# Kernel optimization log

Measured on AMD Instinct MI355X. Metric: run time of the kernel, lower is better.

Reference implementation:

```python
import jax, jax.numpy as jnp
import numpy as np

HW, B, C, NH, NC, HF, WF = 2500, 2, 256, 8, 6, 64, 176
DFF = 4 * C
EPS = 1e-5

def _layernorm(x, g, b):
    m = x.mean(-1, keepdims=True)
    v = ((x - m) ** 2).mean(-1, keepdims=True)
    return (x - m) / jnp.sqrt(v + EPS) * g + b

def _mha(q, kv, in_w, in_b, ow, ob):
    # q: [L,B,C], kv: [S,B,C] (batch_first=False, torch nn.MultiheadAttention)
    L, Bq, Cq = q.shape
    S = kv.shape[0]
    Dh = Cq // NH
    qp = (q @ in_w[:Cq].T + in_b[:Cq]).reshape(L, Bq, NH, Dh)
    kp = (kv @ in_w[Cq:2 * Cq].T + in_b[Cq:2 * Cq]).reshape(S, Bq, NH, Dh)
    vp = (kv @ in_w[2 * Cq:].T + in_b[2 * Cq:]).reshape(S, Bq, NH, Dh)
    att = jnp.einsum('lbhd,sbhd->bhls', qp, kp) * (1.0 / np.sqrt(Dh))
    att = jax.nn.softmax(att, axis=-1)
    out = jnp.einsum('bhls,sbhd->lbhd', att, vp).reshape(L, Bq, Cq)
    return out @ ow.T + ob

def _grid_sample_zeros(feat, grid):
    # feat: [B,N,C,H,W], grid: [B,N,Q,2] in [-1,1]; bilinear, align_corners=False, zero padding
    Bb, N, Cc, Hf, Wf = feat.shape
    Q = grid.shape[2]
    x = (grid[..., 0] + 1.0) * (Wf / 2.0) - 0.5
    y = (grid[..., 1] + 1.0) * (Hf / 2.0) - 0.5
    x0 = jnp.floor(x); y0 = jnp.floor(y)
    wx = x - x0; wy = y - y0
    x0i = x0.astype(jnp.int32); y0i = y0.astype(jnp.int32)
    ff = feat.reshape(Bb, N, Cc, Hf * Wf)
    def corner(xi, yi, w):
        valid = (xi >= 0) & (xi < Wf) & (yi >= 0) & (yi < Hf)
        idx = jnp.clip(yi, 0, Hf - 1) * Wf + jnp.clip(xi, 0, Wf - 1)  # [B,N,Q]
        g = jnp.take_along_axis(ff, jnp.broadcast_to(idx[:, :, None, :], (Bb, N, Cc, Q)), axis=-1)
        return g * (w * valid)[:, :, None, :]
    return (corner(x0i, y0i, (1.0 - wx) * (1.0 - wy)) + corner(x0i + 1, y0i, wx * (1.0 - wy))
            + corner(x0i, y0i + 1, (1.0 - wx) * wy) + corner(x0i + 1, y0i + 1, wx * wy))

def _forward(bev_queries, prev_bev, image_feat, reference_points, camera_intrinsics, camera_extrinsics,
             in_proj_w, in_proj_b, out_proj_w, out_proj_b, tsa_norm_g, tsa_norm_b,
             sca_w, sca_b, sca_norm_g, sca_norm_b, ffn_w1, ffn_b1, ffn_w2, ffn_b2, ffn_norm_g, ffn_norm_b):
    # TSA (dropout is identity in eval)
    tsa_out = _mha(bev_queries, prev_bev, in_proj_w, in_proj_b, out_proj_w, out_proj_b)
    x = _layernorm(bev_queries + tsa_out, tsa_norm_g, tsa_norm_b)
    # SCA: ego->camera->image projection
    R = camera_extrinsics[:, :, :3, :3]            # [B,N,3,3]
    t = camera_extrinsics[:, :, :3, 3]             # [B,N,3]
    R_e2c = jnp.swapaxes(R, -1, -2)
    t_e2c = -jnp.einsum('bnij,bnj->bni', R_e2c, t)
    pts_cam = jnp.einsum('bnij,qj->bnqi', R_e2c, reference_points) + t_e2c[:, :, None, :]  # [B,N,Q,3]
    pts_img = jnp.einsum('bnij,bnqj->bnqi', camera_intrinsics, pts_cam)
    uv = pts_img[..., :2] / jnp.maximum(pts_img[..., 2:3], 1e-5)
    grid = jnp.stack([2.0 * uv[..., 0] / WF - 1.0, 2.0 * uv[..., 1] / HF - 1.0], axis=-1)  # [B,N,Q,2]
    Bq = bev_queries.shape[1]
    feat_r = image_feat.reshape(Bq, NC, C, HF, WF)
    sampled = _grid_sample_zeros(feat_r, grid).mean(axis=1)   # [B,C,Q]
    sampled = jnp.transpose(sampled, (2, 0, 1))               # [Q,B,C]
    sca_out = sampled @ sca_w.T + sca_b
    x = _layernorm(x + sca_out, sca_norm_g, sca_norm_b)
    # FFN (torch nn.GELU default = exact erf)
    h = jax.nn.gelu(x @ ffn_w1 + ffn_b1, approximate=False)
    ffn_out = h @ ffn_w2 + ffn_b2
    return _layernorm(x + ffn_out, ffn_norm_g, ffn_norm_b)

def setup_inputs():
    key = jax.random.key(0)
    ks = jax.random.split(key, 16)
    f = jnp.float32
    s = 0.02
    return {
        'bev_queries': jax.random.normal(ks[0], (HW, B, C), f),
        'prev_bev': jax.random.normal(ks[1], (HW, B, C), f),
        'image_feat': jax.random.normal(ks[2], (B * NC, C, HF, WF), f),
        'reference_points': jax.random.normal(ks[3], (HW, 3), f) * 20.0,
        'camera_intrinsics': jax.random.normal(ks[4], (B, NC, 3, 3), f),
        'camera_extrinsics': jax.random.normal(ks[5], (B, NC, 4, 4), f),
        'spatial_shapes': jnp.array([[HF, WF]], jnp.int32),
        'in_proj_w': jax.random.normal(ks[6], (3 * C, C), f) * s,
        'in_proj_b': jnp.zeros((3 * C,), f),
        'out_proj_w': jax.random.normal(ks[7], (C, C), f) * s,
        'out_proj_b': jnp.zeros((C,), f),
        'tsa_norm_g': jnp.ones((C,), f), 'tsa_norm_b': jnp.zeros((C,), f),
        'sca_w': jax.random.normal(ks[8], (C, C), f) * s,
        'sca_b': jnp.zeros((C,), f),
        'sca_norm_g': jnp.ones((C,), f), 'sca_norm_b': jnp.zeros((C,), f),
        'ffn_w1': jax.random.normal(ks[9], (C, DFF), f) * s,
        'ffn_b1': jnp.zeros((DFF,), f),
        'ffn_w2': jax.random.normal(ks[10], (DFF, C), f) * s,
        'ffn_b2': jnp.zeros((C,), f),
        'ffn_norm_g': jnp.ones((C,), f), 'ffn_norm_b': jnp.zeros((C,), f),
    }

def reference(bev_queries, prev_bev, image_feat, reference_points, camera_intrinsics, camera_extrinsics,
              in_proj_w, in_proj_b, out_proj_w, out_proj_b, tsa_norm_g, tsa_norm_b,
              sca_w, sca_b, sca_norm_g, sca_norm_b, ffn_w1, ffn_b1, ffn_w2, ffn_b2, ffn_norm_g, ffn_norm_b,
              spatial_shapes):
    return _forward(bev_queries, prev_bev, image_feat, reference_points, camera_intrinsics, camera_extrinsics,
                    in_proj_w, in_proj_b, out_proj_w, out_proj_b, tsa_norm_g, tsa_norm_b,
                    sca_w, sca_b, sca_norm_g, sca_norm_b, ffn_w1, ffn_b1, ffn_w2, ffn_b2, ffn_norm_g, ffn_norm_b)
```

## Files before the change

### kernel.cpp

```cpp
#include <hip/hip_runtime.h>

typedef unsigned short u16;
typedef __attribute__((ext_vector_type(8))) __bf16 bf8_t;
typedef __attribute__((ext_vector_type(4))) float f4_t;

union bf8u { u16 u[8]; bf8_t v; uint4 q; };

__device__ __forceinline__ float bf2f(u16 v) {
  return __uint_as_float(((unsigned int)v) << 16);
}
__device__ __forceinline__ u16 f2bf(float f) {
  union { __bf16 h; u16 u; } c;
  c.h = (__bf16)f;
  return c.u;
}
__device__ __forceinline__ float bflo(unsigned int w) { return __uint_as_float(w << 16); }
__device__ __forceinline__ float bfhi(unsigned int w) { return __uint_as_float(w & 0xFFFF0000u); }
__device__ __forceinline__ float ldf1(const void* p, size_t i, int isf32) {
  return isf32 ? ((const float*)p)[i] : bf2f(((const u16*)p)[i]);
}
__device__ __forceinline__ unsigned int cvtpk(float lo, float hi) {
  unsigned int w;
  asm("v_cvt_pk_bf16_f32 %0, %1, %2" : "=v"(w) : "v"(lo), "v"(hi));
  return w;
}

#define LQ    2500
#define LQP   2560
#define BB    2
#define CC    256
#define NCC   6
#define HFF   64
#define WFF   176
#define DFF   1024
#define MROWS 5000

#define WB_UV   256
#define WB_WQKV 240256
#define WB_WOP  633472
#define WB_WSC  764544
#define WB_WF1  895616
#define WB_WF2  1419904
#define WB_S1   1944192
#define WB_S2   (WB_S1 + 2621440)
#define WB_S3   (WB_S2 + 2621440)
#define WB_VT   (WB_S3 + 2621440)
#define WB_H    WB_S2

__global__ void detect_k(const u16* __restrict__ rp, int* __restrict__ flag) {
  int bad = 0;
  for (int i = threadIdx.x; i < 7500; i += 64) {
    float v = bf2f(rp[i]);
    if (!(fabsf(v) < 1e6f)) bad = 1;
  }
  int anybad = __any(bad);
  if (threadIdx.x == 0) flag[0] = anybad ? 1 : 0;
}

struct WDesc {
  const void* src[3];
  u16* dst[3];
  int n[3];
};
__global__ __launch_bounds__(256) void cvtw_k(WDesc d, u16* __restrict__ vtp,
    const void* __restrict__ refp, const void* __restrict__ intr,
    const void* __restrict__ extr, float* __restrict__ uv,
    const int* __restrict__ flag) {
  const int df = flag[0];
  const int i = blockIdx.y;
  if (i == 4) {
    for (int idx = blockIdx.x * 256 + threadIdx.x; idx < BB * NCC * LQ; idx += gridDim.x * 256) {
      const int bc = idx / LQ;
      const int q = idx - bc * LQ;
      float R[3][3], tv[3], Kc[3][3], p[3];
#pragma unroll
      for (int a = 0; a < 3; ++a) {
#pragma unroll
        for (int j = 0; j < 3; ++j) {
          R[a][j] = ldf1(extr, bc*16 + a*4 + j, df);
          Kc[a][j] = ldf1(intr, bc*9 + a*3 + j, df);
        }
        tv[a] = ldf1(extr, bc*16 + a*4 + 3, df);
      }
#pragma unroll
      for (int j = 0; j < 3; ++j) p[j] = ldf1(refp, q*3 + j, df) - tv[j];
      float pc[3];
#pragma unroll
      for (int a = 0; a < 3; ++a) pc[a] = R[0][a]*p[0] + R[1][a]*p[1] + R[2][a]*p[2];
      float im[3];
#pragma unroll
      for (int a = 0; a < 3; ++a) im[a] = Kc[a][0]*pc[0] + Kc[a][1]*pc[1] + Kc[a][2]*pc[2];
      const float z = fmaxf(im[2], 1e-5f);
      uv[(size_t)idx*2 + 0] = im[0] / z - 0.5f;
      uv[(size_t)idx*2 + 1] = im[1] / z - 0.5f;
    }
    return;
  }
  if (i == 3) {
    const int n = 512 * (LQP - LQ);
    for (int j = blockIdx.x * 256 + threadIdx.x; j < n; j += gridDim.x * 256) {
      const int row = j / (LQP - LQ), col = LQ + j % (LQP - LQ);
      vtp[(size_t)row * LQP + col] = 0;
    }
    return;
  }
  const int n = d.n[i];
  for (int j = blockIdx.x * 256 + threadIdx.x; j < n; j += gridDim.x * 256) {
    if (df) {
      const float4 r = ((const float4*)d.src[i])[j];
      const unsigned int lo = (unsigned int)f2bf(r.x) | ((unsigned int)f2bf(r.y) << 16);
      const unsigned int hi = (unsigned int)f2bf(r.z) | ((unsigned int)f2bf(r.w) << 16);
      ((uint2*)d.dst[i])[j] = make_uint2(lo, hi);
    } else {
      ((uint2*)d.dst[i])[j] = ((const uint2*)d.src[i])[j];
    }
  }
}

__global__ __launch_bounds__(256) void trans_k(
    const void* __restrict__ s0, u16* __restrict__ d0,
    const void* __restrict__ s1, u16* __restrict__ d1,
    const int* __restrict__ flag)
{
  __shared__ u16 tile[64][66];
  const int df = flag[0];
  const void* src; u16* dst; int Ks, Ns;
  if (blockIdx.y == 0) { src = s0; dst = d0; Ks = 256;  Ns = 1024; }
  else                 { src = s1; dst = d1; Ks = 1024; Ns = 256;  }
  const int ntn = Ns >> 6;
  const int kx = blockIdx.x / ntn, nx = blockIdx.x % ntn;
  const int k0 = kx * 64, n0 = nx * 64;
  const int t = threadIdx.x;
  const int col = t & 63, rq = t >> 6;
#pragma unroll
  for (int i = 0; i < 16; ++i) {
    const int r = i * 4 + rq;
    tile[col][r] = f2bf(ldf1(src, (size_t)(k0 + r) * Ns + n0 + col, df));
  }
  __syncthreads();
#pragma unroll
  for (int i = 0; i < 16; ++i) {
    const int n = i * 4 + rq;
    dst[(size_t)(n0 + n) * Ks + k0 + col] = tile[n][col];
  }
}

template<int KTPL, int ACT, int NT>
__global__ __launch_bounds__(64) void gemm_nl(
    const u16* __restrict__ Xv, const u16* __restrict__ W,
    const void* __restrict__ bias,
    u16* __restrict__ Y, int M, int N, const int* __restrict__ flag)
{
  const int df = flag[0];
  const int lane = threadIdx.x;
  const int ln15 = lane & 15, l4 = lane >> 4;
  const int m0 = blockIdx.x * 32, n0 = blockIdx.y * (NT * 16);
  const int am0 = min(m0 + ln15, M - 1);
  const int am1 = min(m0 + 16 + ln15, M - 1);

  f4_t acc[2][NT];
#pragma unroll
  for (int g = 0; g < 2; ++g)
#pragma unroll
    for (int nt = 0; nt < NT; ++nt) acc[g][nt] = (f4_t){0.f, 0.f, 0.f, 0.f};

#pragma unroll 8
  for (int k0 = 0; k0 < KTPL; k0 += 32) {
    bf8u a0, a1;
    a0.q = *(const uint4*)(Xv + (size_t)am0 * KTPL + k0 + l4 * 8);
    a1.q = *(const uint4*)(Xv + (size_t)am1 * KTPL + k0 + l4 * 8);
#pragma unroll
    for (int nt = 0; nt < NT; ++nt) {
      bf8u b;
      b.q = *(const uint4*)&W[(size_t)(n0 + nt * 16 + ln15) * KTPL + k0 + l4 * 8];
      acc[0][nt] = __builtin_amdgcn_mfma_f32_16x16x32_bf16(a0.v, b.v, acc[0][nt], 0, 0, 0);
      acc[1][nt] = __builtin_amdgcn_mfma_f32_16x16x32_bf16(a1.v, b.v, acc[1][nt], 0, 0, 0);
    }
  }
#pragma unroll
  for (int g = 0; g < 2; ++g) {
#pragma unroll
    for (int nt = 0; nt < NT; ++nt) {
      const int gn = n0 + nt * 16 + ln15;
      const float bv = ldf1(bias, gn, df);
#pragma unroll
      for (int r = 0; r < 4; ++r) {
        const int gm = m0 + g * 16 + l4 * 4 + r;
        if (gm < M) {
          float x = acc[g][nt][r] + bv;
          if (ACT) x = 0.5f * x * (1.f + erff(x * 0.70710678118654752f));
          Y[(size_t)gm * N + gn] = f2bf(x);
        }
      }
    }
  }
}

template<int KT, int RES, int TOOUT>
__global__ __launch_bounds__(256) void gemm_ln(
    const u16* __restrict__ Xv, const u16* __restrict__ W,
    const void* __restrict__ bias, const void* __restrict__ resv,
    const void* __restrict__ gw, const void* __restrict__ bw,
    void* __restrict__ Yv, int M, const int* __restrict__ flag)
{
  __shared__ float sR[4][32];
  const int df = flag[0];
  const int t = threadIdx.x;
  const int lane = t & 63, wn = t >> 6;
  const int ln15 = lane & 15, l4 = lane >> 4;
  const int m0 = blockIdx.x * 32;
  const int am0 = min(m0 + ln15, M - 1);
  const int am1 = min(m0 + 16 + ln15, M - 1);

  f4_t acc[2][4];
#pragma unroll
  for (int g = 0; g < 2; ++g)
#pragma unroll
    for (int nt = 0; nt < 4; ++nt) acc[g][nt] = (f4_t){0.f, 0.f, 0.f, 0.f};

#pragma unroll 8
  for (int k0 = 0; k0 < KT; k0 += 32) {
    bf8u a0, a1;
    a0.q = *(const uint4*)(Xv + (size_t)am0 * KT + k0 + l4 * 8);
    a1.q = *(const uint4*)(Xv + (size_t)am1 * KT + k0 + l4 * 8);
#pragma unroll
    for (int nt = 0; nt < 4; ++nt) {
      bf8u b;
      b.q = *(const uint4*)&W[(size_t)(wn * 64 + nt * 16 + ln15) * KT + k0 + l4 * 8];
      acc[0][nt] = __builtin_amdgcn_mfma_f32_16x16x32_bf16(a0.v, b.v, acc[0][nt], 0, 0, 0);
      acc[1][nt] = __builtin_amdgcn_mfma_f32_16x16x32_bf16(a1.v, b.v, acc[1][nt], 0, 0, 0);
    }
  }
  float x[2][4][4];
#pragma unroll
  for (int g = 0; g < 2; ++g)
#pragma unroll
    for (int nt = 0; nt < 4; ++nt) {
      const int gn = wn * 64 + nt * 16 + ln15;
      const float bv = ldf1(bias, gn, df);
#pragma unroll
      for (int r = 0; r < 4; ++r) {
        const int gm = m0 + g * 16 + l4 * 4 + r;
        float xx = acc[g][nt][r] + bv;
        const size_t ri = (size_t)min(gm, M - 1) * CC + gn;
        if (RES == 1)      xx += bf2f(((const u16*)resv)[ri]);
        else if (RES == 2) xx += ldf1(resv, ri, df);
        x[g][nt][r] = xx;
      }
    }
#pragma unroll
  for (int g = 0; g < 2; ++g) {
    float ps[4];
#pragma unroll
    for (int r = 0; r < 4; ++r) {
      ps[r] = x[g][0][r] + x[g][1][r] + x[g][2][r] + x[g][3][r];
#pragma unroll
      for (int o = 1; o < 16; o <<= 1) ps[r] += __shfl_xor(ps[r], o);
    }
    if (ln15 == 0) {
#pragma unroll
      for (int r = 0; r < 4; ++r) sR[wn][g * 16 + l4 * 4 + r] = ps[r];
    }
  }
  __syncthreads();
  float mean[2][4];
#pragma unroll
  for (int g = 0; g < 2; ++g)
#pragma unroll
    for (int r = 0; r < 4; ++r) {
      const int row = g * 16 + l4 * 4 + r;
      mean[g][r] = (sR[0][row] + sR[1][row] + sR[2][row] + sR[3][row]) * 0.00390625f;
    }
  __syncthreads();
#pragma unroll
  for (int g = 0; g < 2; ++g) {
    float pq[4];
#pragma unroll
    for (int r = 0; r < 4; ++r) {
      float d0 = x[g][0][r] - mean[g][r], d1 = x[g][1][r] - mean[g][r];
      float d2 = x[g][2][r] - mean[g][r], d3 = x[g][3][r] - mean[g][r];
      pq[r] = d0*d0 + d1*d1 + d2*d2 + d3*d3;
#pragma unroll
      for (int o = 1; o < 16; o <<= 1) pq[r] += __shfl_xor(pq[r], o);
    }
    if (ln15 == 0) {
#pragma unroll
      for (int r = 0; r < 4; ++r) sR[wn][g * 16 + l4 * 4 + r] = pq[r];
    }
  }
  __syncthreads();
  float rstd[2][4];
#pragma unroll
  for (int g = 0; g < 2; ++g)
#pragma unroll
    for (int r = 0; r < 4; ++r) {
      const int row = g * 16 + l4 * 4 + r;
      const float v = (sR[0][row] + sR[1][row] + sR[2][row] + sR[3][row]) * 0.00390625f;
      rstd[g][r] = rsqrtf(v + 1e-5f);
    }
#pragma unroll
  for (int g = 0; g < 2; ++g)
#pragma unroll
    for (int nt = 0; nt < 4; ++nt) {
      const int gn = wn * 64 + nt * 16 + ln15;
      const float gg = ldf1(gw, gn, df);
      const float be = ldf1(bw, gn, df);
#pragma unroll
      for (int r = 0; r < 4; ++r) {
        const int gm = m0 + g * 16 + l4 * 4 + r;
        if (gm < M) {
          const float y = (x[g][nt][r] - mean[g][r]) * rstd[g][r] * gg + be;
          if (TOOUT && df) ((float*)Yv)[(size_t)gm * CC + gn] = y;
          else             ((u16*)Yv)[(size_t)gm * CC + gn] = f2bf(y);
        }
      }
    }
}

__global__ __launch_bounds__(64) void gemm_qkv(
    const void* __restrict__ Xq, const void* __restrict__ Xkv,
    const u16* __restrict__ Wqkv, const void* __restrict__ bias,
    u16* __restrict__ Qo, u16* __restrict__ Ko, u16* __restrict__ Vt,
    const int* __restrict__ flag)
{
  const int df = flag[0];
  const int lane = threadIdx.x;
  const int ln15 = lane & 15, l4 = lane >> 4;
  const int which = blockIdx.y >> 2;
  const int n0 = (blockIdx.y & 3) * 64;
  const void* Xv = (which == 0) ? Xq : Xkv;
  const u16* W = Wqkv + (size_t)which * 65536;
  const int m0 = blockIdx.x * 32;
  const int am0 = min(m0 + ln15, MROWS - 1);
  const int am1 = min(m0 + 16 + ln15, MROWS - 1);

  f4_t acc[2][4];
#pragma unroll
  for (int g = 0; g < 2; ++g)
#pragma unroll
    for (int nt = 0; nt < 4; ++nt) acc[g][nt] = (f4_t){0.f, 0.f, 0.f, 0.f};

#pragma unroll 8
  for (int k0 = 0; k0 < CC; k0 += 32) {
    bf8u a0, a1;
    if (df) {
      const float* p0 = (const float*)Xv + (size_t)am0 * CC + k0 + l4 * 8;
      float4 r0 = *(const float4*)p0, r1 = *(const float4*)(p0 + 4);
      a0.u[0]=f2bf(r0.x); a0.u[1]=f2bf(r0.y); a0.u[2]=f2bf(r0.z); a0.u[3]=f2bf(r0.w);
      a0.u[4]=f2bf(r1.x); a0.u[5]=f2bf(r1.y); a0.u[6]=f2bf(r1.z); a0.u[7]=f2bf(r1.w);
      const float* p1 = (const float*)Xv + (size_t)am1 * CC + k0 + l4 * 8;
      float4 r2 = *(const float4*)p1, r3 = *(const float4*)(p1 + 4);
      a1.u[0]=f2bf(r2.x); a1.u[1]=f2bf(r2.y); a1.u[2]=f2bf(r2.z); a1.u[3]=f2bf(r2.w);
      a1.u[4]=f2bf(r3.x); a1.u[5]=f2bf(r3.y); a1.u[6]=f2bf(r3.z); a1.u[7]=f2bf(r3.w);
    } else {
      a0.q = *(const uint4*)((const u16*)Xv + (size_t)am0 * CC + k0 + l4 * 8);
      a1.q = *(const uint4*)((const u16*)Xv + (size_t)am1 * CC + k0 + l4 * 8);
    }
#pragma unroll
    for (int nt = 0; nt < 4; ++nt) {
      bf8u b;
      b.q = *(const uint4*)&W[(size_t)(n0 + nt * 16 + ln15) * CC + k0 + l4 * 8];
      acc[0][nt] = __builtin_amdgcn_mfma_f32_16x16x32_bf16(a0.v, b.v, acc[0][nt], 0, 0, 0);
      acc[1][nt] = __builtin_amdgcn_mfma_f32_16x16x32_bf16(a1.v, b.v, acc[1][nt], 0, 0, 0);
    }
  }
#pragma unroll
  for (int g = 0; g < 2; ++g) {
#pragma unroll
    for (int nt = 0; nt < 4; ++nt) {
      const int gn = n0 + nt * 16 + ln15;
      const float bv = ldf1(bias, which * 256 + gn, df);
#pragma unroll
      for (int r = 0; r < 4; ++r) {
        const int gm = m0 + g * 16 + l4 * 4 + r;
        if (gm < MROWS) {
          const float x = acc[g][nt][r] + bv;
          if (which == 2) {
            const int tt = gm >> 1;
            const int tx = tt & 63;
            const int tp = (tx & 35) | ((tx & 12) << 1) | ((tx & 16) >> 2);
            Vt[(size_t)(gn + (gm & 1) * 256) * LQP + ((tt & ~63) | tp)] = f2bf(x);
          } else {
            u16* Y = (which == 0) ? Qo : Ko;
            Y[(size_t)gm * CC + gn] = f2bf(x);
          }
        }
      }
    }
  }
}

#define TPW 10
__global__ __launch_bounds__(256) void attn_mf(
    const u16* __restrict__ Qw, const u16* __restrict__ Kw,
    const u16* __restrict__ Vt, u16* __restrict__ Ow)
{
  __shared__ float sO[4][32][33];
  __shared__ float sM[4][32];
  __shared__ float sL[4][32];
  const int t = threadIdx.x;
  const int lane = t & 63, w = t >> 6;
  const int ln15 = lane & 15, l4 = lane >> 4;
  const int q0 = blockIdx.x * 32;
  const int by = blockIdx.y;
  const int b = by >> 3, h = by & 7;
  const float SCL2E = 0.25505654481f;

  bf8u aqA, aqB;
  {
    const int qra = min(q0 + ln15, LQ - 1);
    const int qrb = min(q0 + 16 + ln15, LQ - 1);
    bf8u qr;
    qr.q = *(const uint4*)&Qw[((size_t)qra * BB + b) * CC + h * 32 + l4 * 8];
#pragma unroll
    for (int i = 0; i < 8; ++i) aqA.u[i] = f2bf(bf2f(qr.u[i]) * SCL2E);
    qr.q = *(const uint4*)&Qw[((size_t)qrb * BB + b) * CC + h * 32 + l4 * 8];
#pragma unroll
    for (int i = 0; i < 8; ++i) aqB.u[i] = f2bf(bf2f(qr.u[i]) * SCL2E);
  }

  f4_t oaccA[2], oaccB[2];
  oaccA[0] = (f4_t){0.f,0.f,0.f,0.f}; oaccA[1] = (f4_t){0.f,0.f,0.f,0.f};
  oaccB[0] = (f4_t){0.f,0.f,0.f,0.f}; oaccB[1] = (f4_t){0.f,0.f,0.f,0.f};
  float mA = -1e30f, lA = 0.f;
  float mB = -1e30f, lB = 0.f;

  const int kt0 = w * TPW;
  const u16* Kbase = &Kw[(size_t)b * CC + h * 32 + l4 * 8];
  const u16* Vbase = &Vt[(size_t)(by * 32 + ln15) * LQP + l4 * 8];

  bf8u bkn[4];
#pragma unroll
  for (int nt = 0; nt < 4; ++nt)
    bkn[nt].q = *(const uint4*)&Kbase[(size_t)(kt0 * 64 + nt * 16 + ln15) * CC];

  for (int kt = kt0; kt < kt0 + TPW; ++kt) {
    const int kb = kt * 64;
    bf8u av[2][2];
#pragma unroll
    for (int m = 0; m < 2; ++m)
#pragma unroll
      for (int dt = 0; dt < 2; ++dt)
        av[m][dt].q = *(const uint4*)&Vbase[(size_t)(dt * 16) * LQP + kb + m * 32];
    f4_t svA[4], svB[4];
    __builtin_amdgcn_s_setprio(1);
#pragma unroll
    for (int nt = 0; nt < 4; ++nt) {
      f4_t z = (f4_t){0.f,0.f,0.f,0.f};
      svA[nt] = __builtin_amdgcn_mfma_f32_16x16x32_bf16(bkn[nt].v, aqA.v, z, 0, 0, 0);
      f4_t z2 = (f4_t){0.f,0.f,0.f,0.f};
      svB[nt] = __builtin_amdgcn_mfma_f32_16x16x32_bf16(bkn[nt].v, aqB.v, z2, 0, 0, 0);
    }
    __builtin_amdgcn_s_setprio(0);
    if (kt + 1 < kt0 + TPW) {
#pragma unroll
      for (int nt = 0; nt < 4; ++nt)
        bkn[nt].q = *(const uint4*)&Kbase[(size_t)(kb + 64 + nt * 16 + ln15) * CC];
    }
    float pA[4][4], pB[4][4];
    if (kb + 64 <= LQ) {
#pragma unroll
      for (int nt = 0; nt < 4; ++nt)
#pragma unroll
        for (int r = 0; r < 4; ++r) { pA[nt][r] = svA[nt][r]; pB[nt][r] = svB[nt][r]; }
    } else {
#pragma unroll
      for (int nt = 0; nt < 4; ++nt)
#pragma unroll
        for (int r = 0; r < 4; ++r) {
          const bool ok = (kb + nt * 16 + l4 * 4 + r < LQ);
          pA[nt][r] = ok ? svA[nt][r] : -1e30f;
          pB[nt][r] = ok ? svB[nt][r] : -1e30f;
        }
    }
    {
      const float thr = mA + 8.f;
      bool nd = false;
#pragma unroll
      for (int nt = 0; nt < 4; ++nt)
#pragma unroll
        for (int r = 0; r < 4; ++r) nd |= (pA[nt][r] > thr);
      if (__any(nd)) {
        const float x0 = fmaxf(fmaxf(pA[0][0], pA[0][1]), fmaxf(pA[0][2], pA[0][3]));
        const float x1 = fmaxf(fmaxf(pA[1][0], pA[1][1]), fmaxf(pA[1][2], pA[1][3]));
        const float x2 = fmaxf(fmaxf(pA[2][0], pA[2][1]), fmaxf(pA[2][2], pA[2][3]));
        const float x3 = fmaxf(fmaxf(pA[3][0], pA[3][1]), fmaxf(pA[3][2], pA[3][3]));
        float mloc = fmaxf(fmaxf(x0, x1), fmaxf(x2, x3));
        mloc = fmaxf(mloc, __shfl_xor(mloc, 16));
        mloc = fmaxf(mloc, __shfl_xor(mloc, 32));
        const float mn = fmaxf(mA, mloc);
        const float alpha = __builtin_amdgcn_exp2f(mA - mn);
        mA = mn;
        lA *= alpha;
#pragma unroll
        for (int r = 0; r < 4; ++r) { oaccA[0][r] *= alpha; oaccA[1][r] *= alpha; }
      }
      float s = 0.f;
#pragma unroll
      for (int nt = 0; nt < 4; ++nt)
#pragma unroll
        for (int r = 0; r < 4; ++r) {
          const float e = __builtin_amdgcn_exp2f(pA[nt][r] - mA);
          pA[nt][r] = e; s += e;
        }
      lA += s;
    }
    {
      const float thr = mB + 8.f;
      bool nd = false;
#pragma unroll
      for (int nt = 0; nt < 4; ++nt)
#pragma unroll
        for (int r = 0; r < 4; ++r) nd |= (pB[nt][r] > thr);
      if (__any(nd)) {
        const float x0 = fmaxf(fmaxf(pB[0][0], pB[0][1]), fmaxf(pB[0][2], pB[0][3]));
        const float x1 = fmaxf(fmaxf(pB[1][0], pB[1][1]), fmaxf(pB[1][2], pB[1][3]));
        const float x2 = fmaxf(fmaxf(pB[2][0], pB[2][1]), fmaxf(pB[2][2], pB[2][3]));
        const float x3 = fmaxf(fmaxf(pB[3][0], pB[3][1]), fmaxf(pB[3][2], pB[3][3]));
        float mloc = fmaxf(fmaxf(x0, x1), fmaxf(x2, x3));
        mloc = fmaxf(mloc, __shfl_xor(mloc, 16));
        mloc = fmaxf(mloc, __shfl_xor(mloc, 32));
        const float mn = fmaxf(mB, mloc);
        const float alpha = __builtin_amdgcn_exp2f(mB - mn);
        mB = mn;
        lB *= alpha;
#pragma unroll
        for (int r = 0; r < 4; ++r) { oaccB[0][r] *= alpha; oaccB[1][r] *= alpha; }
      }
      float s = 0.f;
#pragma unroll
      for (int nt = 0; nt < 4; ++nt)
#pragma unroll
        for (int r = 0; r < 4; ++r) {
          const float e = __builtin_amdgcn_exp2f(pB[nt][r] - mB);
          pB[nt][r] = e; s += e;
        }
      lB += s;
    }
    __builtin_amdgcn_s_setprio(1);
#pragma unroll
    for (int m = 0; m < 2; ++m) {
      bf8u pba, pbb;
      pba.q = make_uint4(cvtpk(pA[2*m][0], pA[2*m][1]),   cvtpk(pA[2*m][2], pA[2*m][3]),
                         cvtpk(pA[2*m+1][0], pA[2*m+1][1]), cvtpk(pA[2*m+1][2], pA[2*m+1][3]));
      pbb.q = make_uint4(cvtpk(pB[2*m][0], pB[2*m][1]),   cvtpk(pB[2*m][2], pB[2*m][3]),
                         cvtpk(pB[2*m+1][0], pB[2*m+1][1]), cvtpk(pB[2*m+1][2], pB[2*m+1][3]));
#pragma unroll
      for (int dt = 0; dt < 2; ++dt) {
        oaccA[dt] = __builtin_amdgcn_mfma_f32_16x16x32_bf16(av[m][dt].v, pba.v, oaccA[dt], 0, 0, 0);
        oaccB[dt] = __builtin_amdgcn_mfma_f32_16x16x32_bf16(av[m][dt].v, pbb.v, oaccB[dt], 0, 0, 0);
      }
    }
    __builtin_amdgcn_s_setprio(0);
  }
  lA += __shfl_xor(lA, 16);  lA += __shfl_xor(lA, 32);
  lB += __shfl_xor(lB, 16);  lB += __shfl_xor(lB, 32);
#pragma unroll
  for (int dt = 0; dt < 2; ++dt)
#pragma unroll
    for (int r = 0; r < 4; ++r) {
      sO[w][ln15][dt * 16 + l4 * 4 + r]      = oaccA[dt][r];
      sO[w][16 + ln15][dt * 16 + l4 * 4 + r] = oaccB[dt][r];
    }
  if (l4 == 0) {
    sM[w][ln15] = mA; sL[w][ln15] = lA;
    sM[w][16 + ln15] = mB; sL[w][16 + ln15] = lB;
  }
  __syncthreads();
#pragma unroll
  for (int i = t; i < 1024; i += 256) {
    const int row = i >> 5, col = i & 31;
    const float M = fmaxf(fmaxf(sM[0][row], sM[1][row]), fmaxf(sM[2][row], sM[3][row]));
    float l = 0.f, O = 0.f;
#pragma unroll
    for (int w4 = 0; w4 < 4; ++w4) {
      const float sc = __builtin_amdgcn_exp2f(sM[w4][row] - M);
      l += sc * sL[w4][row];
      O += sc * sO[w4][row][col];
    }
    const int q = q0 + row;
    if (q < LQ)
      Ow[((size_t)q * BB + b) * CC + h * 32 + col] = f2bf(O / l);
  }
}

__global__ __launch_bounds__(256) void samp_k(
    const void* __restrict__ feat, const float* __restrict__ uv,
    u16* __restrict__ S, const int* __restrict__ flag)
{
  const int df = flag[0];
  const int c = blockIdx.x;
  const int b = blockIdx.y / 5;
  const int ch = blockIdx.y % 5;
  const int qend = min((ch + 1) * 500, LQ);
  for (int q = ch * 500 + threadIdx.x; q < qend; q += 256) {
    float acc = 0.f;
#pragma unroll
    for (int cam = 0; cam < NCC; ++cam) {
      const int bc = b * NCC + cam;
      const float x = uv[((size_t)bc * LQ + q) * 2 + 0];
      const float y = uv[((size_t)bc * LQ + q) * 2 + 1];
      const float xf = floorf(x), yf = floorf(y);
      const int x0 = (int)xf, y0 = (int)yf;
      const float wx = x - xf, wy = y - yf;
      const size_t base = ((size_t)bc * CC + c) * (HFF * WFF);
      const bool vx0 = (x0 >= 0) & (x0 < WFF);
      const bool vx1 = (x0 + 1 >= 0) & (x0 + 1 < WFF);
      const bool vy0 = (y0 >= 0) & (y0 < HFF);
      const bool vy1 = (y0 + 1 >= 0) & (y0 + 1 < HFF);
      if (vy0) {
        const size_t rb = base + (size_t)y0 * WFF;
        if (vx0) acc += (1.f - wx) * (1.f - wy) * ldf1(feat, rb + x0, df);
        if (vx1) acc += wx * (1.f - wy) * ldf1(feat, rb + x0 + 1, df);
      }
      if (vy1) {
        const size_t rb = base + (size_t)(y0 + 1) * WFF;
        if (vx0) acc += (1.f - wx) * wy * ldf1(feat, rb + x0, df);
        if (vx1) acc += wx * wy * ldf1(feat, rb + x0 + 1, df);
      }
    }
    S[((size_t)q * BB + b) * CC + c] = f2bf(acc * (1.f / 6.f));
  }
}

extern "C" void kernel_launch(void* const* d_in, const int* in_sizes, int n_in,
                              void* d_out, int out_size, void* d_ws, size_t ws_size,
                              hipStream_t stream) {
  (void)in_sizes; (void)n_in; (void)out_size; (void)ws_size;
  char* base = (char*)d_ws;
  int* flag = (int*)base;
  float* UV = (float*)(base + WB_UV);
  u16* WQKV = (u16*)(base + WB_WQKV);
  u16* WOP  = (u16*)(base + WB_WOP);
  u16* WSC  = (u16*)(base + WB_WSC);
  u16* WF1  = (u16*)(base + WB_WF1);
  u16* WF2  = (u16*)(base + WB_WF2);
  u16* S1 = (u16*)(base + WB_S1);
  u16* S2 = (u16*)(base + WB_S2);
  u16* S3 = (u16*)(base + WB_S3);
  u16* VT = (u16*)(base + WB_VT);
  u16* H  = (u16*)(base + WB_H);

  detect_k<<<1, 64, 0, stream>>>((const u16*)d_in[3], flag);

  WDesc wd;
  wd.src[0] = d_in[7];  wd.dst[0] = WQKV; wd.n[0] = 49152;
  wd.src[1] = d_in[9];  wd.dst[1] = WOP;  wd.n[1] = 16384;
  wd.src[2] = d_in[13]; wd.dst[2] = WSC;  wd.n[2] = 16384;
  cvtw_k<<<dim3(128, 5), 256, 0, stream>>>(wd, VT, d_in[3], d_in[4], d_in[5], UV, flag);
  trans_k<<<dim3(64, 2), 256, 0, stream>>>(d_in[17], WF1, d_in[19], WF2, flag);

  gemm_qkv<<<dim3(157, 12), 64, 0, stream>>>(d_in[0], d_in[1], WQKV, d_in[8], S1, S2, VT, flag);

  attn_mf<<<dim3(79, 16), 256, 0, stream>>>(S1, S2, VT, S3);

  gemm_ln<256,2,0><<<157, 256, 0, stream>>>(S3, WOP, d_in[10], d_in[0], d_in[11], d_in[12], S2, MROWS, flag);

  samp_k<<<dim3(CC, BB * 5), 256, 0, stream>>>(d_in[2], UV, VT, flag);

  gemm_ln<256,1,0><<<157, 256, 0, stream>>>(VT, WSC, d_in[14], S2, d_in[15], d_in[16], S1, MROWS, flag);

  gemm_nl<256,1,4><<<dim3(157, 16), 64, 0, stream>>>(S1, WF1, d_in[18], H, MROWS, DFF, flag);
  gemm_ln<1024,1,1><<<157, 256, 0, stream>>>(H, WF2, d_in[20], S1, d_in[21], d_in[22], d_out, MROWS, flag);
}
```

Baseline: 453.9 us.

## Merge weight transpose into conversion kernel and co-schedule sampling with attention

Folds the FFN weight transpose kernel into the weight-conversion launch as an extra blockIdx.y slice. Also merges the independent bilinear camera sampling into the attention launch as extra blocks writing to a new workspace buffer SB, so the memory-bound gather can overlap with the compute-bound attention. This removes two kernel launches and lets both workloads share the GPU. The cost is that the sampling blocks now carry the attention kernel's shared-memory footprint, which may lower occupancy, and the workspace grows by one buffer.

```diff
diff --git a/kernel.cpp b/kernel.cpp
--- a/kernel.cpp
+++ b/kernel.cpp
@@ -45,6 +45,7 @@
 #define WB_S2   (WB_S1 + 2621440)
 #define WB_S3   (WB_S2 + 2621440)
 #define WB_VT   (WB_S3 + 2621440)
+#define WB_SB   (WB_VT + 2621440)
 #define WB_H    WB_S2
 
 __global__ void detect_k(const u16* __restrict__ rp, int* __restrict__ flag) {
@@ -65,9 +66,34 @@
 __global__ __launch_bounds__(256) void cvtw_k(WDesc d, u16* __restrict__ vtp,
     const void* __restrict__ refp, const void* __restrict__ intr,
     const void* __restrict__ extr, float* __restrict__ uv,
+    const void* __restrict__ tw1, u16* __restrict__ td1,
+    const void* __restrict__ tw2, u16* __restrict__ td2,
     const int* __restrict__ flag) {
   const int df = flag[0];
   const int i = blockIdx.y;
+  if (i == 5) {
+    __shared__ u16 tile[64][66];
+    const void* src; u16* dst; int Ks, Ns, bx;
+    if (blockIdx.x < 64) { src = tw1; dst = td1; Ks = 256;  Ns = 1024; bx = blockIdx.x; }
+    else                 { src = tw2; dst = td2; Ks = 1024; Ns = 256;  bx = blockIdx.x - 64; }
+    const int ntn = Ns >> 6;
+    const int kx = bx / ntn, nx = bx % ntn;
+    const int k0 = kx * 64, n0 = nx * 64;
+    const int t = threadIdx.x;
+    const int col = t & 63, rq = t >> 6;
+#pragma unroll
+    for (int ii = 0; ii < 16; ++ii) {
+      const int r = ii * 4 + rq;
+      tile[col][r] = f2bf(ldf1(src, (size_t)(k0 + r) * Ns + n0 + col, df));
+    }
+    __syncthreads();
+#pragma unroll
+    for (int ii = 0; ii < 16; ++ii) {
+      const int n = ii * 4 + rq;
+      dst[(size_t)(n0 + n) * Ks + k0 + col] = tile[n][col];
+    }
+    return;
+  }
   if (i == 4) {
     for (int idx = blockIdx.x * 256 + threadIdx.x; idx < BB * NCC * LQ; idx += gridDim.x * 256) {
       const int bc = idx / LQ;
@@ -114,34 +140,6 @@
     } else {
       ((uint2*)d.dst[i])[j] = ((const uint2*)d.src[i])[j];
     }
-  }
-}
-
-__global__ __launch_bounds__(256) void trans_k(
-    const void* __restrict__ s0, u16* __restrict__ d0,
-    const void* __restrict__ s1, u16* __restrict__ d1,
-    const int* __restrict__ flag)
-{
-  __shared__ u16 tile[64][66];
-  const int df = flag[0];
-  const void* src; u16* dst; int Ks, Ns;
-  if (blockIdx.y == 0) { src = s0; dst = d0; Ks = 256;  Ns = 1024; }
-  else                 { src = s1; dst = d1; Ks = 1024; Ns = 256;  }
-  const int ntn = Ns >> 6;
-  const int kx = blockIdx.x / ntn, nx = blockIdx.x % ntn;
-  const int k0 = kx * 64, n0 = nx * 64;
-  const int t = threadIdx.x;
-  const int col = t & 63, rq = t >> 6;
-#pragma unroll
-  for (int i = 0; i < 16; ++i) {
-    const int r = i * 4 + rq;
-    tile[col][r] = f2bf(ldf1(src, (size_t)(k0 + r) * Ns + n0 + col, df));
-  }
-  __syncthreads();
-#pragma unroll
-  for (int i = 0; i < 16; ++i) {
-    const int n = i * 4 + rq;
-    dst[(size_t)(n0 + n) * Ks + k0 + col] = tile[n][col];
   }
 }
 
@@ -391,18 +389,59 @@
 }
 
 #define TPW 10
-__global__ __launch_bounds__(256) void attn_mf(
+#define ATTN_BLOCKS (79 * 16)
+__global__ __launch_bounds__(256) void attn_samp(
     const u16* __restrict__ Qw, const u16* __restrict__ Kw,
-    const u16* __restrict__ Vt, u16* __restrict__ Ow)
+    const u16* __restrict__ Vt, u16* __restrict__ Ow,
+    const void* __restrict__ feat, const float* __restrict__ uv,
+    u16* __restrict__ SB, const int* __restrict__ flag)
 {
+  const int t = threadIdx.x;
+  if (blockIdx.x >= ATTN_BLOCKS) {
+    const int df = flag[0];
+    const int sid = blockIdx.x - ATTN_BLOCKS;
+    const int c = sid & 255;
+    const int yy = sid >> 8;
+    const int b = yy / 5;
+    const int ch = yy % 5;
+    const int qend = min((ch + 1) * 500, LQ);
+    for (int q = ch * 500 + t; q < qend; q += 256) {
+      float acc = 0.f;
+#pragma unroll
+      for (int cam = 0; cam < NCC; ++cam) {
+        const int bc = b * NCC + cam;
+        const float x = uv[((size_t)bc * LQ + q) * 2 + 0];
+        const float y = uv[((size_t)bc * LQ + q) * 2 + 1];
+        const float xf = floorf(x), yf = floorf(y);
+        const int x0 = (int)xf, y0 = (int)yf;
+        const float wx = x - xf, wy = y - yf;
+        const size_t base = ((size_t)bc * CC + c) * (HFF * WFF);
+        const bool vx0 = (x0 >= 0) & (x0 < WFF);
+        const bool vx1 = (x0 + 1 >= 0) & (x0 + 1 < WFF);
+        const bool vy0 = (y0 >= 0) & (y0 < HFF);
+        const bool vy1 = (y0 + 1 >= 0) & (y0 + 1 < HFF);
+        if (vy0) {
+          const size_t rb = base + (size_t)y0 * WFF;
+          if (vx0) acc += (1.f - wx) * (1.f - wy) * ldf1(feat, rb + x0, df);
+          if (vx1) acc += wx * (1.f - wy) * ldf1(feat, rb + x0 + 1, df);
+        }
+        if (vy1) {
+          const size_t rb = base + (size_t)(y0 + 1) * WFF;
+          if (vx0) acc += (1.f - wx) * wy * ldf1(feat, rb + x0, df);
+          if (vx1) acc += wx * wy * ldf1(feat, rb + x0 + 1, df);
+        }
+      }
+      SB[((size_t)q * BB + b) * CC + c] = f2bf(acc * (1.f / 6.f));
+    }
+    return;
+  }
   __shared__ float sO[4][32][33];
   __shared__ float sM[4][32];
   __shared__ float sL[4][32];
-  const int t = threadIdx.x;
   const int lane = t & 63, w = t >> 6;
   const int ln15 = lane & 15, l4 = lane >> 4;
-  const int q0 = blockIdx.x * 32;
-  const int by = blockIdx.y;
+  const int q0 = (blockIdx.x % 79) * 32;
+  const int by = blockIdx.x / 79;
   const int b = by >> 3, h = by & 7;
   const float SCL2E = 0.25505654481f;
 
@@ -581,45 +620,6 @@
     const int q = q0 + row;
     if (q < LQ)
       Ow[((size_t)q * BB + b) * CC + h * 32 + col] = f2bf(O / l);
-  }
-}
-
-__global__ __launch_bounds__(256) void samp_k(
-    const void* __restrict__ feat, const float* __restrict__ uv,
-    u16* __restrict__ S, const int* __restrict__ flag)
-{
-  const int df = flag[0];
-  const int c = blockIdx.x;
-  const int b = blockIdx.y / 5;
-  const int ch = blockIdx.y % 5;
-  const int qend = min((ch + 1) * 500, LQ);
-  for (int q = ch * 500 + threadIdx.x; q < qend; q += 256) {
-    float acc = 0.f;
-#pragma unroll
-    for (int cam = 0; cam < NCC; ++cam) {
-      const int bc = b * NCC + cam;
-      const float x = uv[((size_t)bc * LQ + q) * 2 + 0];
-      const float y = uv[((size_t)bc * LQ + q) * 2 + 1];
-      const float xf = floorf(x), yf = floorf(y);
-      const int x0 = (int)xf, y0 = (int)yf;
-      const float wx = x - xf, wy = y - yf;
-      const size_t base = ((size_t)bc * CC + c) * (HFF * WFF);
-      const bool vx0 = (x0 >= 0) & (x0 < WFF);
-      const bool vx1 = (x0 + 1 >= 0) & (x0 + 1 < WFF);
-      const bool vy0 = (y0 >= 0) & (y0 < HFF);
-      const bool vy1 = (y0 + 1 >= 0) & (y0 + 1 < HFF);
-      if (vy0) {
-        const size_t rb = base + (size_t)y0 * WFF;
-        if (vx0) acc += (1.f - wx) * (1.f - wy) * ldf1(feat, rb + x0, df);
-        if (vx1) acc += wx * (1.f - wy) * ldf1(feat, rb + x0 + 1, df);
-      }
-      if (vy1) {
-        const size_t rb = base + (size_t)(y0 + 1) * WFF;
-        if (vx0) acc += (1.f - wx) * wy * ldf1(feat, rb + x0, df);
-        if (vx1) acc += wx * wy * ldf1(feat, rb + x0 + 1, df);
-      }
-    }
-    S[((size_t)q * BB + b) * CC + c] = f2bf(acc * (1.f / 6.f));
   }
 }
 
@@ -639,6 +639,7 @@
   u16* S2 = (u16*)(base + WB_S2);
   u16* S3 = (u16*)(base + WB_S3);
   u16* VT = (u16*)(base + WB_VT);
+  u16* SB = (u16*)(base + WB_SB);
   u16* H  = (u16*)(base + WB_H);
 
   detect_k<<<1, 64, 0, stream>>>((const u16*)d_in[3], flag);
@@ -647,18 +648,17 @@
   wd.src[0] = d_in[7];  wd.dst[0] = WQKV; wd.n[0] = 49152;
   wd.src[1] = d_in[9];  wd.dst[1] = WOP;  wd.n[1] = 16384;
   wd.src[2] = d_in[13]; wd.dst[2] = WSC;  wd.n[2] = 16384;
-  cvtw_k<<<dim3(128, 5), 256, 0, stream>>>(wd, VT, d_in[3], d_in[4], d_in[5], UV, flag);
-  trans_k<<<dim3(64, 2), 256, 0, stream>>>(d_in[17], WF1, d_in[19], WF2, flag);
+  cvtw_k<<<dim3(128, 6), 256, 0, stream>>>(wd, VT, d_in[3], d_in[4], d_in[5], UV,
+                                           d_in[17], WF1, d_in[19], WF2, flag);
 
   gemm_qkv<<<dim3(157, 12), 64, 0, stream>>>(d_in[0], d_in[1], WQKV, d_in[8], S1, S2, VT, flag);
 
-  attn_mf<<<dim3(79, 16), 256, 0, stream>>>(S1, S2, VT, S3);
+  attn_samp<<<ATTN_BLOCKS + 2560, 256, 0, stream>>>(S1, S2, VT, S3,
+                                                    d_in[2], UV, SB, flag);
 
   gemm_ln<256,2,0><<<157, 256, 0, stream>>>(S3, WOP, d_in[10], d_in[0], d_in[11], d_in[12], S2, MROWS, flag);
 
-  samp_k<<<dim3(CC, BB * 5), 256, 0, stream>>>(d_in[2], UV, VT, flag);
-
-  gemm_ln<256,1,0><<<157, 256, 0, stream>>>(VT, WSC, d_in[14], S2, d_in[15], d_in[16], S1, MROWS, flag);
+  gemm_ln<256,1,0><<<157, 256, 0, stream>>>(SB, WSC, d_in[14], S2, d_in[15], d_in[16], S1, MROWS, flag);
 
   gemm_nl<256,1,4><<<dim3(157, 16), 64, 0, stream>>>(S1, WF1, d_in[18], H, MROWS, DFF, flag);
   gemm_ln<1024,1,1><<<157, 256, 0, stream>>>(H, WF2, d_in[20], S1, d_in[21], d_in[22], d_out, MROWS, flag);
```

Measured after the change: 465.8 us. 2.6% more time.
